# Kernel optimization log

Hardware: AMD Instinct MI355X
Metric: run time of the kernel (lower is better)

Reference implementation:

```python
import jax, jax.numpy as jnp
import numpy as np

EPS = 1e-6
SIGMA = 1.0       # get_matrix default sigma
INIT_SIGMA = 1.0  # args.init_sigma


def setup_inputs() -> dict:
    key = jax.random.key(0)
    ks = jax.random.split(key, 12)
    B, T, LD, NB = 16, 2048, 256, 32
    s = 1.0 / np.sqrt(LD)
    E_raw = jax.random.normal(ks[5], (LD, LD), jnp.float32)
    E_w, _ = jnp.linalg.qr(E_raw)  # orthogonal like geotorch.orthogonal
    return {
        "Z": jax.random.normal(ks[0], (B, T, LD), jnp.float32),
        "obs_times": jax.random.uniform(ks[1], (B, T, 1), jnp.float32),
        "D": jax.random.normal(ks[2], (NB, LD), jnp.float32),
        "coeff_W": jax.random.normal(ks[3], (NB, LD), jnp.float32) * s,
        "coeff_b": jnp.zeros((NB,), jnp.float32),
        "E_w": E_w.astype(jnp.float32),
        "B_w": jax.random.normal(ks[6], (LD, LD), jnp.float32) * s,
        "C_w": jax.random.normal(ks[7], (LD, LD), jnp.float32) * s,
        "M_w": jax.random.normal(ks[8], (LD, LD), jnp.float32) * s,
        "init_mean_p": jax.random.normal(ks[9], (LD,), jnp.float32),
        "init_log_var": jax.random.normal(ks[10], (LD,), jnp.float32),
        "y_log_var": jax.random.normal(ks[11], (LD,), jnp.float32),
    }


def _binop(qi, qj):
    # (A_j*A_i, Bu_j + A_j*Bu_i): combine earlier element qi with later qj
    A_i, Bu_i = qi
    A_j, Bu_j = qj
    return (A_j * A_i, Bu_j + A_j * Bu_i)


def reference(Z, obs_times, D, coeff_W, coeff_b, E_w, B_w, C_w, M_w,
              init_mean_p, init_log_var, y_log_var):
    LD = Z.shape[-1]
    # alphas = B(Z)
    alphas = jnp.einsum('btd,ed->bte', Z, B_w)                      # (B,T,LD)
    # get_matrix (vectorized over batch and time)
    A_basis = -(jnp.exp(D) + EPS)                                   # (NB,LD), negative
    A_coeff = jax.nn.softmax(jnp.einsum('btd,nd->btn', alphas, coeff_W) + coeff_b, axis=-1)
    A_mat = jnp.einsum('btn,nd->btd', A_coeff, A_basis)             # (B,T,LD)
    exp_A_m = jnp.exp(A_mat * obs_times)                            # mean transition
    exp_B_m = (exp_A_m - 1.0) / A_mat * alphas
    exp_A_v = jnp.exp(2.0 * A_mat * obs_times)                      # var transition
    exp_B_v = 0.5 * SIGMA ** 2 * (exp_A_v - 1.0) / A_mat + EPS
    mats_A = jnp.concatenate([exp_A_m, exp_A_v], axis=-1)           # (B,T,2LD)
    mats_B = jnp.concatenate([exp_B_m, exp_B_v], axis=-1)           # (B,T,2LD)
    # parallel linear-recurrence scan over time
    cum_A, cum_B = jax.lax.associative_scan(_binop, (mats_A, mats_B), axis=1)
    # initial condition in rotated coordinates
    init_mean0 = E_w.T @ init_mean_p                                # (LD,)
    diag_v = INIT_SIGMA * (jnp.exp(init_log_var) + EPS)
    init_var0 = jnp.einsum('ki,k->i', E_w ** 2, diag_v)             # diag(E^T diag(v) E)
    init_mv = jnp.concatenate([init_mean0, init_var0], axis=0)      # (2LD,)
    imv = cum_A * init_mv                                           # (B,T,2LD)
    init_mean, init_var = imv[..., :LD], imv[..., LD:]
    xs_mean, xs_var = cum_B[..., :LD], cum_B[..., LD:]
    y_var = jnp.exp(y_log_var) + EPS
    # output projections: M(E(.)) and history C(E(Z))
    history = jnp.einsum('btd,ed,fe->btf', Z, E_w, C_w)
    means = jnp.einsum('btd,ed,fe->btf', xs_mean + init_mean, E_w, M_w) + history
    stds = jnp.einsum('btd,ed,fe->btf', jnp.sqrt(xs_var + init_var + y_var), E_w, M_w)
    return means, stds, alphas
```

## Files before the change

kernel.cpp:

```cpp
#include <hip/hip_runtime.h>
#include <math.h>

#define EPS 1e-6f

#define B_   16
#define T_   2048
#define LD   256
#define NB   32
#define BT   (B_ * T_)
#define NCH  32
#define CHUNK (T_ / NCH)

typedef short bf16x8 __attribute__((ext_vector_type(8)));
typedef float f32x4  __attribute__((ext_vector_type(4)));

__device__ __forceinline__ unsigned short f2b(float f) {
    unsigned int u = __float_as_uint(f);
    unsigned int r = (u + 0x7fffu + ((u >> 16) & 1u)) >> 16;
    return (unsigned short)r;
}

__device__ __forceinline__ void gl_lds16(const void* g, void* l) {
    __builtin_amdgcn_global_load_lds(
        (const __attribute__((address_space(1))) unsigned int*)g,
        (__attribute__((address_space(3))) unsigned int*)l, 16, 0, 0);
}

__device__ __forceinline__ void stage_tile(const unsigned short* __restrict__ src,
                                           int row0, int stride, int kb,
                                           unsigned short* lds, int wv, int lane) {
#pragma unroll
    for (int cc = 0; cc < 2; ++cc) {
        int c = wv * 2 + cc;
        int r = c * 16 + (lane >> 2);
        int qd = (lane & 3) ^ ((r >> 1) & 3);
        const unsigned short* g = src + (size_t)(row0 + r) * stride + kb + qd * 8;
        gl_lds16(g, lds + c * 512);
    }
}

__device__ __forceinline__ bf16x8 frag_ld(const unsigned short* lds, int row, int qd) {
    int pq = qd ^ ((row >> 1) & 3);
    return *(const bf16x8*)(lds + row * 32 + pq * 8);
}

__global__ __launch_bounds__(256) void k_pre(const float* __restrict__ Z,
                                             const float* __restrict__ Dm,
                                             const float* __restrict__ cw,
                                             const float* __restrict__ Ew,
                                             const float* __restrict__ Bw,
                                             const float* __restrict__ Cw,
                                             const float* __restrict__ Mw,
                                             const float* __restrict__ imp,
                                             const float* __restrict__ ilv,
                                             const float* __restrict__ ylv,
                                             unsigned short* __restrict__ GMh,
                                             unsigned short* __restrict__ GCh,
                                             unsigned short* __restrict__ cwbh,
                                             float* __restrict__ im0,
                                             float* __restrict__ iv0,
                                             float* __restrict__ yv,
                                             float* __restrict__ Ab,
                                             unsigned short* __restrict__ Bwh,
                                             unsigned short* __restrict__ Zh) {
    int bid = blockIdx.x;
    int tid = threadIdx.x;
    if (bid < 544) {
        const float* W; const float* E; unsigned short* out; int d0, f0;
        if (bid < 256)      { W = Mw; E = Ew; out = GMh;  d0 = (bid & 15) * 16; f0 = (bid >> 4) * 16; }
        else if (bid < 512) { W = Cw; E = Ew; out = GCh;  d0 = (bid & 15) * 16; f0 = ((bid - 256) >> 4) * 16; }
        else                { W = cw; E = Bw; out = cwbh; d0 = (bid & 15) * 16; f0 = ((bid - 512) >> 4) * 16; }
        __shared__ float Ws[16][17];
        __shared__ float Es[16][17];
        int tx = tid & 15, ty = tid >> 4;
        float acc = 0.f;
        for (int eb = 0; eb < LD; eb += 16) {
            Ws[ty][tx] = W[(f0 + ty) * LD + eb + tx];
            Es[ty][tx] = E[(eb + ty) * LD + d0 + tx];
            __syncthreads();
#pragma unroll
            for (int k = 0; k < 16; ++k) acc = fmaf(Ws[ty][k], Es[k][tx], acc);
            __syncthreads();
        }
        out[(f0 + ty) * LD + d0 + tx] = f2b(acc);
    } else if (bid < 577) {
        int sub = bid - 544;
        int t = tid;
        if (sub == 0) {
            float sm = 0.f, sv = 0.f;
            for (int k = 0; k < LD; ++k) {
                float e = Ew[k * LD + t];
                sm = fmaf(e, imp[k], sm);
                sv = fmaf(e * e, expf(ilv[k]) + EPS, sv);
            }
            im0[t] = sm;
            iv0[t] = sv;
            yv[t]  = expf(ylv[t]) + EPS;
        } else {
            int n = sub - 1;
            Ab[n * LD + t] = -(expf(Dm[n * LD + t]) + EPS);
        }
    } else if (bid < 641) {
        int i = (bid - 577) * 256 + tid;
        float4 v = ((const float4*)Bw)[i];
        ((ushort4*)Bwh)[i] = make_ushort4(f2b(v.x), f2b(v.y), f2b(v.z), f2b(v.w));
    } else {
        int i = (bid - 641) * 256 + tid;
        float4 v = ((const float4*)Z)[i];
        ((ushort4*)Zh)[i] = make_ushort4(f2b(v.x), f2b(v.y), f2b(v.z), f2b(v.w));
    }
}

__global__ __launch_bounds__(256) void k_zb(const unsigned short* __restrict__ Zh,
                                            const unsigned short* __restrict__ Bwh,
                                            const unsigned short* __restrict__ cwbh,
                                            const float* __restrict__ cb,
                                            float* __restrict__ alphas,
                                            float* __restrict__ logits) {
    __shared__ unsigned short As[128 * 32];
    __shared__ unsigned short Bs[128 * 32];
    int tid = threadIdx.x, lane = tid & 63, wv = tid >> 6;
    int m0 = blockIdx.x * 128;
    int y  = blockIdx.y;
    if (y < 2) {
        int n0 = y * 128;
        int wm = (wv & 1) * 64, wn = (wv >> 1) * 64;
        f32x4 acc[4][4];
#pragma unroll
        for (int i = 0; i < 4; ++i)
#pragma unroll
            for (int j = 0; j < 4; ++j) acc[i][j] = (f32x4){0.f, 0.f, 0.f, 0.f};
        for (int kb = 0; kb < LD; kb += 32) {
            stage_tile(Zh, m0, LD, kb, As, wv, lane);
            stage_tile(Bwh, n0, LD, kb, Bs, wv, lane);
            __syncthreads();
            int qd = lane >> 4;
            bf16x8 af[4], bf[4];
#pragma unroll
            for (int i = 0; i < 4; ++i) af[i] = frag_ld(As, wm + i * 16 + (lane & 15), qd);
#pragma unroll
            for (int j = 0; j < 4; ++j) bf[j] = frag_ld(Bs, wn + j * 16 + (lane & 15), qd);
#pragma unroll
            for (int i = 0; i < 4; ++i)
#pragma unroll
                for (int j = 0; j < 4; ++j)
                    acc[i][j] = __builtin_amdgcn_mfma_f32_16x16x32_bf16(af[i], bf[j], acc[i][j], 0, 0, 0);
            __syncthreads();
        }
        int col = wn + (lane & 15);
        int rb  = wm + ((lane >> 4) << 2);
#pragma unroll
        for (int i = 0; i < 4; ++i)
#pragma unroll
            for (int j = 0; j < 4; ++j)
#pragma unroll
                for (int r = 0; r < 4; ++r)
                    alphas[(size_t)(m0 + rb + i * 16 + r) * LD + n0 + col + j * 16] = acc[i][j][r];
    } else {
        f32x4 acc[2][2];
#pragma unroll
        for (int i = 0; i < 2; ++i)
#pragma unroll
            for (int j = 0; j < 2; ++j) acc[i][j] = (f32x4){0.f, 0.f, 0.f, 0.f};
        for (int kb = 0; kb < LD; kb += 32) {
            stage_tile(Zh, m0, LD, kb, As, wv, lane);
            if (wv < 2) {
                int r = wv * 16 + (lane >> 2);
                int qd = (lane & 3) ^ ((r >> 1) & 3);
                gl_lds16(cwbh + (size_t)r * LD + kb + qd * 8, Bs + wv * 512);
            }
            __syncthreads();
            int qd = lane >> 4;
            bf16x8 af[2], bff[2];
#pragma unroll
            for (int i = 0; i < 2; ++i) af[i] = frag_ld(As, wv * 32 + i * 16 + (lane & 15), qd);
#pragma unroll
            for (int j = 0; j < 2; ++j) bff[j] = frag_ld(Bs, j * 16 + (lane & 15), qd);
#pragma unroll
            for (int i = 0; i < 2; ++i)
#pragma unroll
                for (int j = 0; j < 2; ++j)
                    acc[i][j] = __builtin_amdgcn_mfma_f32_16x16x32_bf16(af[i], bff[j], acc[i][j], 0, 0, 0);
            __syncthreads();
        }
        int col = lane & 15;
        int rb  = (lane >> 4) << 2;
#pragma unroll
        for (int i = 0; i < 2; ++i)
#pragma unroll
            for (int j = 0; j < 2; ++j)
#pragma unroll
                for (int r = 0; r < 4; ++r) {
                    int row = m0 + wv * 32 + i * 16 + rb + r;
                    int cc  = j * 16 + col;
                    logits[(size_t)row * NB + cc] = acc[i][j][r] + cb[cc];
                }
    }
}

__device__ __forceinline__ void scan_prolog(const float* __restrict__ logits,
                                            const float* __restrict__ obs,
                                            const float* __restrict__ Ab,
                                            int bt0, int d,
                                            float (*lg)[NB], float* obs_s, float* abc) {
    int tid = threadIdx.x;
    float4* lg4 = (float4*)lg;
    const float4* g4 = (const float4*)(logits + (size_t)bt0 * NB);
    lg4[tid]       = g4[tid];
    lg4[tid + 256] = g4[tid + 256];
    if (tid < CHUNK) obs_s[tid] = obs[bt0 + tid];
    __syncthreads();
    int l = tid & 31, rg = tid >> 5;
#pragma unroll
    for (int j = 0; j < 8; ++j) {
        int row = rg * 8 + j;
        float v = lg[row][l];
        float mx = v;
#pragma unroll
        for (int off = 16; off >= 1; off >>= 1) mx = fmaxf(mx, __shfl_xor(mx, off, 32));
        float e = expf(v - mx);
        float s = e;
#pragma unroll
        for (int off = 16; off >= 1; off >>= 1) s += __shfl_xor(s, off, 32);
        lg[row][l] = e / s;
    }
    __syncthreads();
#pragma unroll
    for (int n = 0; n < NB; ++n) abc[n] = Ab[n * LD + d];
}

__global__ __launch_bounds__(256) void k_tot(const float* __restrict__ logits,
                                             const float* __restrict__ alphas,
                                             const float* __restrict__ obs,
                                             const float* __restrict__ Ab,
                                             float* __restrict__ totA,
                                             float* __restrict__ totBm,
                                             float* __restrict__ totBv) {
    __shared__ float lg[CHUNK][NB];
    __shared__ float obs_s[CHUNK];
    int d = threadIdx.x;
    int b = blockIdx.x >> 5, ch = blockIdx.x & 31;
    int bt0 = b * T_ + ch * CHUNK;
    float abc[NB];
    scan_prolog(logits, obs, Ab, bt0, d, lg, obs_s, abc);
    float ra = 1.f, rm = 0.f, rv = 0.f;
    for (int i = 0; i < CHUNK; ++i) {
        float av = alphas[(size_t)(bt0 + i) * LD + d];
        float Am = 0.f;
#pragma unroll
        for (int n = 0; n < NB; ++n) Am = fmaf(lg[i][n], abc[n], Am);
        float tt  = obs_s[i];
        float eAm = expf(Am * tt);
        float ieA = 1.f / Am;
        float eBm = (eAm - 1.f) * ieA * av;
        float eBv = 0.5f * (eAm * eAm - 1.f) * ieA + EPS;
        rm = fmaf(eAm, rm, eBm);
        rv = fmaf(eAm * eAm, rv, eBv);
        ra *= eAm;
    }
    int pidx = blockIdx.x * LD + d;
    totA[pidx] = ra; totBm[pidx] = rm; totBv[pidx] = rv;
}

__global__ void k_chunkpfx(const float* __restrict__ totA, const float* __restrict__ totBm,
                           const float* __restrict__ totBv,
                           float* __restrict__ preA, float* __restrict__ preBm,
                           float* __restrict__ preBv) {
    int d = threadIdx.x;
    int b = blockIdx.x;
    float Pa = 1.f, Pm = 0.f, Pv = 0.f;
    for (int ch = 0; ch < NCH; ++ch) {
        int pidx = (b * NCH + ch) * LD + d;
        preA[pidx] = Pa; preBm[pidx] = Pm; preBv[pidx] = Pv;
        float a = totA[pidx], tm_ = totBm[pidx], tv = totBv[pidx];
        Pm = fmaf(a, Pm, tm_);
        Pv = fmaf(a * a, Pv, tv);
        Pa = a * Pa;
    }
}

__global__ __launch_bounds__(256) void k_scan_apply(const float* __restrict__ logits,
                                                    const float* __restrict__ alphas,
                                                    const float* __restrict__ obs,
                                                    const float* __restrict__ Ab,
                                                    const float* __restrict__ preA,
                                                    const float* __restrict__ preBm,
                                                    const float* __restrict__ preBv,
                                                    const float* __restrict__ im0,
                                                    const float* __restrict__ iv0,
                                                    const float* __restrict__ yv,
                                                    unsigned short* __restrict__ Mh,
                                                    unsigned short* __restrict__ Sh) {
    __shared__ float lg[CHUNK][NB];
    __shared__ float obs_s[CHUNK];
    int d = threadIdx.x;
    int b = blockIdx.x >> 5, ch = blockIdx.x & 31;
    int bt0 = b * T_ + ch * CHUNK;
    float abc[NB];
    scan_prolog(logits, obs, Ab, bt0, d, lg, obs_s, abc);
    int pidx = blockIdx.x * LD + d;
    float ga = preA[pidx], gm = preBm[pidx], gv = preBv[pidx];
    float i0 = im0[d], v0 = iv0[d], yvd = yv[d];
    for (int i = 0; i < CHUNK; ++i) {
        size_t idx = (size_t)(bt0 + i) * LD + d;
        float av = alphas[idx];
        float Am = 0.f;
#pragma unroll
        for (int n = 0; n < NB; ++n) Am = fmaf(lg[i][n], abc[n], Am);
        float tt  = obs_s[i];
        float eAm = expf(Am * tt);
        float ieA = 1.f / Am;
        float eBm = (eAm - 1.f) * ieA * av;
        float eBv = 0.5f * (eAm * eAm - 1.f) * ieA + EPS;
        gm = fmaf(eAm, gm, eBm);
        gv = fmaf(eAm * eAm, gv, eBv);
        ga *= eAm;
        float mm = fmaf(ga, i0, gm);
        float vv = fmaf(ga * ga, v0, gv) + yvd;
        Mh[idx] = f2b(mm);
        Sh[idx] = f2b(sqrtf(vv));
    }
}

__global__ __launch_bounds__(256) void k_ms(const unsigned short* __restrict__ Mh,
                                            const unsigned short* __restrict__ Zh,
                                            const unsigned short* __restrict__ Sh,
                                            const unsigned short* __restrict__ GMh,
                                            const unsigned short* __restrict__ GCh,
                                            float* __restrict__ means,
                                            float* __restrict__ stds) {
    __shared__ unsigned short As[128 * 32];
    __shared__ unsigned short Bs[128 * 32];
    int tid = threadIdx.x, lane = tid & 63, wv = tid >> 6;
    int m0 = blockIdx.x * 128;
    int y  = blockIdx.y;
    int halves = (y < 2) ? 2 : 1;
    int n0 = (y < 2) ? y * 128 : (y - 2) * 128;
    const unsigned short* A0 = (y < 2) ? Mh : Sh;
    const unsigned short* A1 = Zh;
    const unsigned short* B0 = GMh;
    const unsigned short* B1 = GCh;
    float* C = (y < 2) ? means : stds;
    int wm = (wv & 1) * 64, wn = (wv >> 1) * 64;
    f32x4 acc[4][4];
#pragma unroll
    for (int i = 0; i < 4; ++i)
#pragma unroll
        for (int j = 0; j < 4; ++j) acc[i][j] = (f32x4){0.f, 0.f, 0.f, 0.f};
    for (int h = 0; h < halves; ++h) {
        const unsigned short* A = h ? A1 : A0;
        const unsigned short* B = h ? B1 : B0;
        for (int kb = 0; kb < LD; kb += 32) {
            stage_tile(A, m0, LD, kb, As, wv, lane);
            stage_tile(B, n0, LD, kb, Bs, wv, lane);
            __syncthreads();
            int qd = lane >> 4;
            bf16x8 af[4], bf[4];
#pragma unroll
            for (int i = 0; i < 4; ++i) af[i] = frag_ld(As, wm + i * 16 + (lane & 15), qd);
#pragma unroll
            for (int j = 0; j < 4; ++j) bf[j] = frag_ld(Bs, wn + j * 16 + (lane & 15), qd);
#pragma unroll
            for (int i = 0; i < 4; ++i)
#pragma unroll
                for (int j = 0; j < 4; ++j)
                    acc[i][j] = __builtin_amdgcn_mfma_f32_16x16x32_bf16(af[i], bf[j], acc[i][j], 0, 0, 0);
            __syncthreads();
        }
    }
    int col = wn + (lane & 15);
    int rb  = wm + ((lane >> 4) << 2);
#pragma unroll
    for (int i = 0; i < 4; ++i)
#pragma unroll
        for (int j = 0; j < 4; ++j)
#pragma unroll
            for (int r = 0; r < 4; ++r)
                C[(size_t)(m0 + rb + i * 16 + r) * LD + n0 + col + j * 16] = acc[i][j][r];
}

extern "C" void kernel_launch(void* const* d_in, const int* in_sizes, int n_in,
                              void* d_out, int out_size, void* d_ws, size_t ws_size,
                              hipStream_t stream) {
    const float* Z   = (const float*)d_in[0];
    const float* obs = (const float*)d_in[1];
    const float* Dm  = (const float*)d_in[2];
    const float* cw  = (const float*)d_in[3];
    const float* cb  = (const float*)d_in[4];
    const float* Ew  = (const float*)d_in[5];
    const float* Bw  = (const float*)d_in[6];
    const float* Cw  = (const float*)d_in[7];
    const float* Mw  = (const float*)d_in[8];
    const float* imp = (const float*)d_in[9];
    const float* ilv = (const float*)d_in[10];
    const float* ylv = (const float*)d_in[11];

    float* out    = (float*)d_out;
    float* means  = out;
    float* stds   = out + (size_t)BT * LD;
    float* alphas = out + (size_t)2 * BT * LD;

    char* ws = (char*)d_ws;
    size_t o = 0;
    unsigned short* Zh   = (unsigned short*)(ws + o); o += (size_t)BT * LD * 2;
    unsigned short* Mh   = (unsigned short*)(ws + o); o += (size_t)BT * LD * 2;
    unsigned short* Sh   = (unsigned short*)(ws + o); o += (size_t)BT * LD * 2;
    float*          logits=(float*)(ws + o);          o += (size_t)BT * NB * 4;
    unsigned short* GMh  = (unsigned short*)(ws + o); o += (size_t)LD * LD * 2;
    unsigned short* GCh  = (unsigned short*)(ws + o); o += (size_t)LD * LD * 2;
    unsigned short* Bwh  = (unsigned short*)(ws + o); o += (size_t)LD * LD * 2;
    unsigned short* cwbh = (unsigned short*)(ws + o); o += (size_t)NB * LD * 2;
    float* Ab    = (float*)(ws + o); o += (size_t)NB * LD * 4;
    float* totA  = (float*)(ws + o); o += (size_t)B_ * NCH * LD * 4;
    float* totBm = (float*)(ws + o); o += (size_t)B_ * NCH * LD * 4;
    float* totBv = (float*)(ws + o); o += (size_t)B_ * NCH * LD * 4;
    float* preA  = (float*)(ws + o); o += (size_t)B_ * NCH * LD * 4;
    float* preBm = (float*)(ws + o); o += (size_t)B_ * NCH * LD * 4;
    float* preBv = (float*)(ws + o); o += (size_t)B_ * NCH * LD * 4;
    float* im0   = (float*)(ws + o); o += LD * 4;
    float* iv0   = (float*)(ws + o); o += LD * 4;
    float* yv    = (float*)(ws + o); o += LD * 4;

    k_pre<<<dim3(641 + BT * LD / 1024), dim3(256), 0, stream>>>(
        Z, Dm, cw, Ew, Bw, Cw, Mw, imp, ilv, ylv,
        GMh, GCh, cwbh, im0, iv0, yv, Ab, Bwh, Zh);

    k_zb<<<dim3(BT / 128, 3), dim3(256), 0, stream>>>(Zh, Bwh, cwbh, cb, alphas, logits);

    k_tot<<<dim3(B_ * NCH), dim3(LD), 0, stream>>>(logits, alphas, obs, Ab, totA, totBm, totBv);
    k_chunkpfx<<<dim3(B_), dim3(LD), 0, stream>>>(totA, totBm, totBv, preA, preBm, preBv);
    k_scan_apply<<<dim3(B_ * NCH), dim3(LD), 0, stream>>>(logits, alphas, obs, Ab,
                                                          preA, preBm, preBv,
                                                          im0, iv0, yv, Mh, Sh);

    k_ms<<<dim3(BT / 128, 4), dim3(256), 0, stream>>>(Mh, Zh, Sh, GMh, GCh, means, stds);
}
```

Measured before the change: 249.3 us.

## Fuse scan-apply with output projection GEMM and halve chunk size

Merges the scan-apply kernel and the mean/std projection GEMM into one kernel that keeps the bf16 scan results for a 32-step chunk in LDS and multiplies them directly by the projection weights. This removes the global round-trip of the Mh/Sh intermediates and one launch. The chunk count doubles to 64 so the fused kernel has enough blocks and its LDS tiles fit. In exchange the weight tiles are re-staged once per 32-row chunk, and the per-chunk GEMM tiles are small.

```diff
diff --git a/kernel.cpp b/kernel.cpp
--- a/kernel.cpp
+++ b/kernel.cpp
@@ -8,7 +8,7 @@
 #define LD   256
 #define NB   32
 #define BT   (B_ * T_)
-#define NCH  32
+#define NCH  64
 #define CHUNK (T_ / NCH)
 
 typedef short bf16x8 __attribute__((ext_vector_type(8)));
@@ -35,6 +35,18 @@
         int r = c * 16 + (lane >> 2);
         int qd = (lane & 3) ^ ((r >> 1) & 3);
         const unsigned short* g = src + (size_t)(row0 + r) * stride + kb + qd * 8;
+        gl_lds16(g, lds + c * 512);
+    }
+}
+
+__device__ __forceinline__ void stage_tile256(const unsigned short* __restrict__ src,
+                                              int kb, unsigned short* lds, int wv, int lane) {
+#pragma unroll
+    for (int cc = 0; cc < 4; ++cc) {
+        int c = wv * 4 + cc;
+        int r = c * 16 + (lane >> 2);
+        int qd = (lane & 3) ^ ((r >> 1) & 3);
+        const unsigned short* g = src + (size_t)r * LD + kb + qd * 8;
         gl_lds16(g, lds + c * 512);
     }
 }
@@ -206,14 +218,13 @@
     int tid = threadIdx.x;
     float4* lg4 = (float4*)lg;
     const float4* g4 = (const float4*)(logits + (size_t)bt0 * NB);
-    lg4[tid]       = g4[tid];
-    lg4[tid + 256] = g4[tid + 256];
+    lg4[tid] = g4[tid];
     if (tid < CHUNK) obs_s[tid] = obs[bt0 + tid];
     __syncthreads();
     int l = tid & 31, rg = tid >> 5;
 #pragma unroll
-    for (int j = 0; j < 8; ++j) {
-        int row = rg * 8 + j;
+    for (int j = 0; j < CHUNK / 8; ++j) {
+        int row = rg * (CHUNK / 8) + j;
         float v = lg[row][l];
         float mx = v;
 #pragma unroll
@@ -239,8 +250,7 @@
     __shared__ float lg[CHUNK][NB];
     __shared__ float obs_s[CHUNK];
     int d = threadIdx.x;
-    int b = blockIdx.x >> 5, ch = blockIdx.x & 31;
-    int bt0 = b * T_ + ch * CHUNK;
+    int bt0 = blockIdx.x * CHUNK;
     float abc[NB];
     scan_prolog(logits, obs, Ab, bt0, d, lg, obs_s, abc);
     float ra = 1.f, rm = 0.f, rv = 0.f;
@@ -279,31 +289,39 @@
     }
 }
 
-__global__ __launch_bounds__(256) void k_scan_apply(const float* __restrict__ logits,
-                                                    const float* __restrict__ alphas,
-                                                    const float* __restrict__ obs,
-                                                    const float* __restrict__ Ab,
-                                                    const float* __restrict__ preA,
-                                                    const float* __restrict__ preBm,
-                                                    const float* __restrict__ preBv,
-                                                    const float* __restrict__ im0,
-                                                    const float* __restrict__ iv0,
-                                                    const float* __restrict__ yv,
-                                                    unsigned short* __restrict__ Mh,
-                                                    unsigned short* __restrict__ Sh) {
-    __shared__ float lg[CHUNK][NB];
-    __shared__ float obs_s[CHUNK];
-    int d = threadIdx.x;
-    int b = blockIdx.x >> 5, ch = blockIdx.x & 31;
-    int bt0 = b * T_ + ch * CHUNK;
+__global__ __launch_bounds__(256) void k_sms(const float* __restrict__ logits,
+                                             const float* __restrict__ alphas,
+                                             const float* __restrict__ obs,
+                                             const float* __restrict__ Ab,
+                                             const float* __restrict__ preA,
+                                             const float* __restrict__ preBm,
+                                             const float* __restrict__ preBv,
+                                             const float* __restrict__ im0,
+                                             const float* __restrict__ iv0,
+                                             const float* __restrict__ yv,
+                                             const unsigned short* __restrict__ Zh,
+                                             const unsigned short* __restrict__ GMh,
+                                             const unsigned short* __restrict__ GCh,
+                                             float* __restrict__ means,
+                                             float* __restrict__ stds) {
+    __shared__ unsigned short Ms[CHUNK * LD];
+    __shared__ unsigned short Ss[CHUNK * LD];
+    __shared__ unsigned short Bs[256 * 32];
+    float (*lg)[NB] = (float(*)[NB])Bs;
+    float* obs_s = (float*)(Bs + 2048 + 2048);
+
+    int tid = threadIdx.x, lane = tid & 63, wv = tid >> 6;
+    int d = tid;
+    int bt0 = blockIdx.x * CHUNK;
     float abc[NB];
     scan_prolog(logits, obs, Ab, bt0, d, lg, obs_s, abc);
+
     int pidx = blockIdx.x * LD + d;
     float ga = preA[pidx], gm = preBm[pidx], gv = preBv[pidx];
     float i0 = im0[d], v0 = iv0[d], yvd = yv[d];
+    int dc = d >> 5, q = (d & 31) >> 3, jj = d & 7;
     for (int i = 0; i < CHUNK; ++i) {
-        size_t idx = (size_t)(bt0 + i) * LD + d;
-        float av = alphas[idx];
+        float av = alphas[(size_t)(bt0 + i) * LD + d];
         float Am = 0.f;
 #pragma unroll
         for (int n = 0; n < NB; ++n) Am = fmaf(lg[i][n], abc[n], Am);
@@ -317,66 +335,78 @@
         ga *= eAm;
         float mm = fmaf(ga, i0, gm);
         float vv = fmaf(ga * ga, v0, gv) + yvd;
-        Mh[idx] = f2b(mm);
-        Sh[idx] = f2b(sqrtf(vv));
-    }
-}
-
-__global__ __launch_bounds__(256) void k_ms(const unsigned short* __restrict__ Mh,
-                                            const unsigned short* __restrict__ Zh,
-                                            const unsigned short* __restrict__ Sh,
-                                            const unsigned short* __restrict__ GMh,
-                                            const unsigned short* __restrict__ GCh,
-                                            float* __restrict__ means,
-                                            float* __restrict__ stds) {
-    __shared__ unsigned short As[128 * 32];
-    __shared__ unsigned short Bs[128 * 32];
-    int tid = threadIdx.x, lane = tid & 63, wv = tid >> 6;
-    int m0 = blockIdx.x * 128;
-    int y  = blockIdx.y;
-    int halves = (y < 2) ? 2 : 1;
-    int n0 = (y < 2) ? y * 128 : (y - 2) * 128;
-    const unsigned short* A0 = (y < 2) ? Mh : Sh;
-    const unsigned short* A1 = Zh;
-    const unsigned short* B0 = GMh;
-    const unsigned short* B1 = GCh;
-    float* C = (y < 2) ? means : stds;
-    int wm = (wv & 1) * 64, wn = (wv >> 1) * 64;
-    f32x4 acc[4][4];
-#pragma unroll
-    for (int i = 0; i < 4; ++i)
-#pragma unroll
-        for (int j = 0; j < 4; ++j) acc[i][j] = (f32x4){0.f, 0.f, 0.f, 0.f};
-    for (int h = 0; h < halves; ++h) {
-        const unsigned short* A = h ? A1 : A0;
-        const unsigned short* B = h ? B1 : B0;
-        for (int kb = 0; kb < LD; kb += 32) {
-            stage_tile(A, m0, LD, kb, As, wv, lane);
-            stage_tile(B, n0, LD, kb, Bs, wv, lane);
-            __syncthreads();
-            int qd = lane >> 4;
-            bf16x8 af[4], bf[4];
-#pragma unroll
-            for (int i = 0; i < 4; ++i) af[i] = frag_ld(As, wm + i * 16 + (lane & 15), qd);
-#pragma unroll
-            for (int j = 0; j < 4; ++j) bf[j] = frag_ld(Bs, wn + j * 16 + (lane & 15), qd);
-#pragma unroll
-            for (int i = 0; i < 4; ++i)
-#pragma unroll
-                for (int j = 0; j < 4; ++j)
-                    acc[i][j] = __builtin_amdgcn_mfma_f32_16x16x32_bf16(af[i], bf[j], acc[i][j], 0, 0, 0);
-            __syncthreads();
-        }
-    }
-    int col = wn + (lane & 15);
-    int rb  = wm + ((lane >> 4) << 2);
-#pragma unroll
-    for (int i = 0; i < 4; ++i)
+        int pq = q ^ ((i >> 1) & 3);
+        int a = dc * (CHUNK * 32) + i * 32 + pq * 8 + jj;
+        Ms[a] = f2b(mm);
+        Ss[a] = f2b(sqrtf(vv));
+    }
+    __syncthreads();
+
+    f32x4 accm[2][4], accs[2][4];
+#pragma unroll
+    for (int i = 0; i < 2; ++i)
+#pragma unroll
+        for (int j = 0; j < 4; ++j) {
+            accm[i][j] = (f32x4){0.f, 0.f, 0.f, 0.f};
+            accs[i][j] = (f32x4){0.f, 0.f, 0.f, 0.f};
+        }
+    int qd = lane >> 4, mr = lane & 15;
+    for (int kc = 0; kc < 8; ++kc) {
+        stage_tile256(GMh, kc * 32, Bs, wv, lane);
+        __syncthreads();
+        bf16x8 am[2], as[2], bfr[4];
+#pragma unroll
+        for (int i = 0; i < 2; ++i) {
+            int row = i * 16 + mr;
+            int pq = qd ^ ((row >> 1) & 3);
+            am[i] = *(const bf16x8*)(Ms + kc * (CHUNK * 32) + row * 32 + pq * 8);
+            as[i] = *(const bf16x8*)(Ss + kc * (CHUNK * 32) + row * 32 + pq * 8);
+        }
+#pragma unroll
+        for (int j = 0; j < 4; ++j) bfr[j] = frag_ld(Bs, wv * 64 + j * 16 + mr, qd);
+#pragma unroll
+        for (int i = 0; i < 2; ++i)
+#pragma unroll
+            for (int j = 0; j < 4; ++j) {
+                accm[i][j] = __builtin_amdgcn_mfma_f32_16x16x32_bf16(am[i], bfr[j], accm[i][j], 0, 0, 0);
+                accs[i][j] = __builtin_amdgcn_mfma_f32_16x16x32_bf16(as[i], bfr[j], accs[i][j], 0, 0, 0);
+            }
+        __syncthreads();
+    }
+
+    for (int kc = 0; kc < 8; ++kc) {
+        stage_tile256(GCh, kc * 32, Bs, wv, lane);
+        if (wv < 2) {
+            int r = wv * 16 + (lane >> 2);
+            int qz = (lane & 3) ^ ((r >> 1) & 3);
+            gl_lds16(Zh + (size_t)(bt0 + r) * LD + kc * 32 + qz * 8, Ss + wv * 512);
+        }
+        __syncthreads();
+        bf16x8 az[2], bfr[4];
+#pragma unroll
+        for (int i = 0; i < 2; ++i) az[i] = frag_ld(Ss, i * 16 + mr, qd);
+#pragma unroll
+        for (int j = 0; j < 4; ++j) bfr[j] = frag_ld(Bs, wv * 64 + j * 16 + mr, qd);
+#pragma unroll
+        for (int i = 0; i < 2; ++i)
+#pragma unroll
+            for (int j = 0; j < 4; ++j)
+                accm[i][j] = __builtin_amdgcn_mfma_f32_16x16x32_bf16(az[i], bfr[j], accm[i][j], 0, 0, 0);
+        __syncthreads();
+    }
+
+    int col0 = wv * 64 + mr;
+    int rb   = (lane >> 4) << 2;
+#pragma unroll
+    for (int i = 0; i < 2; ++i)
 #pragma unroll
         for (int j = 0; j < 4; ++j)
 #pragma unroll
-            for (int r = 0; r < 4; ++r)
-                C[(size_t)(m0 + rb + i * 16 + r) * LD + n0 + col + j * 16] = acc[i][j][r];
+            for (int r = 0; r < 4; ++r) {
+                size_t off = (size_t)(bt0 + i * 16 + rb + r) * LD + col0 + j * 16;
+                means[off] = accm[i][j][r];
+                stds[off]  = accs[i][j][r];
+            }
 }
 
 extern "C" void kernel_launch(void* const* d_in, const int* in_sizes, int n_in,
@@ -403,8 +433,6 @@
     char* ws = (char*)d_ws;
     size_t o = 0;
     unsigned short* Zh   = (unsigned short*)(ws + o); o += (size_t)BT * LD * 2;
-    unsigned short* Mh   = (unsigned short*)(ws + o); o += (size_t)BT * LD * 2;
-    unsigned short* Sh   = (unsigned short*)(ws + o); o += (size_t)BT * LD * 2;
     float*          logits=(float*)(ws + o);          o += (size_t)BT * NB * 4;
     unsigned short* GMh  = (unsigned short*)(ws + o); o += (size_t)LD * LD * 2;
     unsigned short* GCh  = (unsigned short*)(ws + o); o += (size_t)LD * LD * 2;
@@ -429,9 +457,9 @@
 
     k_tot<<<dim3(B_ * NCH), dim3(LD), 0, stream>>>(logits, alphas, obs, Ab, totA, totBm, totBv);
     k_chunkpfx<<<dim3(B_), dim3(LD), 0, stream>>>(totA, totBm, totBv, preA, preBm, preBv);
-    k_scan_apply<<<dim3(B_ * NCH), dim3(LD), 0, stream>>>(logits, alphas, obs, Ab,
-                                                          preA, preBm, preBv,
-                                                          im0, iv0, yv, Mh, Sh);
-
-    k_ms<<<dim3(BT / 128, 4), dim3(256), 0, stream>>>(Mh, Zh, Sh, GMh, GCh, means, stds);
-}
+
+    k_sms<<<dim3(B_ * NCH), dim3(256), 0, stream>>>(logits, alphas, obs, Ab,
+                                                    preA, preBm, preBv,
+                                                    im0, iv0, yv,
+                                                    Zh, GMh, GCh, means, stds);
+}
```

After: 244.5 us. No clear change (-1.9%).
